# Optimization experiments

Measured on AMD Instinct MI355X. Metric: run time of the kernel, lower is better.

Reference implementation:

```python
import jax, jax.numpy as jnp
import numpy as np

N = 100000   # nodes
E = 1600000  # edges (before self-loops)
IN = 128     # in_dim
H = 32       # hidden (hardcoded in module)
G = 2048     # graphs in batch
NEG_SLOPE = 0.2  # PyG GATConv default leaky_relu slope


def setup_inputs() -> dict:
    key = jax.random.key(0)
    ks = jax.random.split(key, 20)
    inp = {
        "x": jax.random.normal(ks[0], (N, IN), jnp.float32),
        "edge_index": jax.random.randint(ks[1], (2, E), 0, N, dtype=jnp.int64),
        "batch": jnp.sort(jax.random.randint(ks[2], (N,), 0, G, dtype=jnp.int64)),
    }
    dims = [(IN, H), (H, H), (H, H), (H, H)]
    for i, (di, do) in enumerate(dims, start=1):
        k = 3 + 4 * (i - 1)
        inp[f"W{i}"] = jax.random.normal(ks[k], (di, do), jnp.float32) * 0.1
        inp[f"a_s{i}"] = jax.random.normal(ks[k + 1], (do,), jnp.float32) * 0.1
        inp[f"a_d{i}"] = jax.random.normal(ks[k + 2], (do,), jnp.float32) * 0.1
        inp[f"b{i}"] = jnp.zeros((do,), jnp.float32)
    return inp


def _gat(x, src, dst, W, a_s, a_d, b):
    # PyG GATConv, heads=1: h = xW; e_ij = leaky_relu(a_s.h_j + a_d.h_i);
    # alpha = softmax over incoming edges of i; out_i = sum_j alpha_ij * h_j + b
    h = x @ W                                # [N, H]
    es = h @ a_s                             # [N]
    ed = h @ a_d                             # [N]
    e = jax.nn.leaky_relu(es[src] + ed[dst], NEG_SLOPE)   # [E+N]
    m = jax.ops.segment_max(e, dst, num_segments=N)        # per-dest max (stable softmax)
    ex = jnp.exp(e - m[dst])
    denom = jax.ops.segment_sum(ex, dst, num_segments=N)
    alpha = ex / denom[dst]
    out = jax.ops.segment_sum(alpha[:, None] * h[src], dst, num_segments=N)
    return out + b


def reference(x, edge_index, batch, W1, a_s1, a_d1, b1, W2, a_s2, a_d2, b2,
              W3, a_s3, a_d3, b3, W4, a_s4, a_d4, b4):
    # add self-loops once (GATConv add_self_loops=True; same edge set every layer)
    loop = jnp.arange(N, dtype=edge_index.dtype)
    src = jnp.concatenate([edge_index[0], loop])
    dst = jnp.concatenate([edge_index[1], loop])
    x = _gat(x, src, dst, W1, a_s1, a_d1, b1)  # tanh in source is a no-op (result discarded)
    x = _gat(x, src, dst, W2, a_s2, a_d2, b2)
    x = _gat(x, src, dst, W3, a_s3, a_d3, b3)
    x = _gat(x, src, dst, W4, a_s4, a_d4, b4)
    # global_mean_pool
    sums = jax.ops.segment_sum(x, batch, num_segments=G)
    cnt = jax.ops.segment_sum(jnp.ones((N,), x.dtype), batch, num_segments=G)
    return sums / jnp.maximum(cnt, 1.0)[:, None]
```

## Files before the change

### kernel.cpp

```cpp
#include <hip/hip_runtime.h>
#include <hip/hip_fp16.h>

#define HDIM 32
#define IN_DIM 128
#define NEG_SLOPE 0.2f
#define NPB 128
#define NPB_SHIFT 7
#define MAXB 1024
#define CHUNK 8192
#define CAP 4096

typedef _Float16 half8  __attribute__((ext_vector_type(8)));
typedef _Float16 half4v __attribute__((ext_vector_type(4)));
typedef float    floatx4 __attribute__((ext_vector_type(4)));
typedef float    floatx2 __attribute__((ext_vector_type(2)));

__device__ __forceinline__ float leaky(float e) {
    return (e >= 0.f) ? e : NEG_SLOPE * e;
}


template<int K>
__global__ __launch_bounds__(256) void gemm_f32in(
    const float* __restrict__ x, const float* __restrict__ W,
    const float* __restrict__ a_s, const float* __restrict__ a_d,
    uint2* __restrict__ h8, float* __restrict__ es, float* __restrict__ ed, int N)
{
    constexpr int KP = K + 8;
    __shared__ _Float16 xs[64 * KP];
    __shared__ _Float16 Wt[32 * KP];
    __shared__ float stage[64 * 33];
    const int tid = threadIdx.x;
    for (int i = tid; i < K * 32; i += 256) {
        int k = i >> 5, n = i & 31;
        Wt[n * KP + k] = (_Float16)W[i];
    }
    const int lane = tid & 63;
    const int wave = tid >> 6;
    const int m16  = lane & 15;
    const int quad = lane >> 4;
    const float as0 = a_s[m16], as1 = a_s[m16 + 16];
    const float ad0 = a_d[m16], ad1 = a_d[m16 + 16];

    const int ntiles = (N + 63) >> 6;
    for (int tile = blockIdx.x; tile < ntiles; tile += gridDim.x) {
        const int row0 = tile << 6;
        __syncthreads();
        for (int i = tid; i < 64 * (K / 4); i += 256) {
            int r  = i / (K / 4);
            int c4 = i % (K / 4);
            float4 v = (row0 + r < N) ? ((const float4*)x)[(size_t)(row0 + r) * (K / 4) + c4]
                                      : make_float4(0.f, 0.f, 0.f, 0.f);
            half4v hv = { (_Float16)v.x, (_Float16)v.y, (_Float16)v.z, (_Float16)v.w };
            *(half4v*)&xs[r * KP + c4 * 4] = hv;
        }
        __syncthreads();
        floatx4 acc0 = {0.f, 0.f, 0.f, 0.f}, acc1 = {0.f, 0.f, 0.f, 0.f};
        const int rbase = wave * 16;
        #pragma unroll
        for (int kt = 0; kt < K / 32; kt++) {
            half8 a  = *(half8*)&xs[(rbase + m16) * KP + kt * 32 + quad * 8];
            half8 b0 = *(half8*)&Wt[m16 * KP + kt * 32 + quad * 8];
            half8 b1 = *(half8*)&Wt[(m16 + 16) * KP + kt * 32 + quad * 8];
            acc0 = __builtin_amdgcn_mfma_f32_16x16x32_f16(a, b0, acc0, 0, 0, 0);
            acc1 = __builtin_amdgcn_mfma_f32_16x16x32_f16(a, b1, acc1, 0, 0, 0);
        }
        #pragma unroll
        for (int r = 0; r < 4; r++) {
            const int lr = rbase + quad * 4 + r;
            int row = row0 + lr;
            float c0 = acc0[r], c1 = acc1[r];
            stage[lr * 33 + m16]      = c0;
            stage[lr * 33 + m16 + 16] = c1;
            float ps = c0 * as0 + c1 * as1;
            float pd = c0 * ad0 + c1 * ad1;
            #pragma unroll
            for (int m = 8; m >= 1; m >>= 1) { ps += __shfl_xor(ps, m); pd += __shfl_xor(pd, m); }
            if (row < N && m16 == 0) { es[row] = ps; ed[row] = pd; }
        }
        __syncthreads();
        {
            int r = tid >> 2, seg = tid & 3;
            int row = row0 + r;
            if (row < N) {
                const float* sp = &stage[r * 33 + seg * 8];
                unsigned int u0, u1;
                u0 = __builtin_amdgcn_cvt_pk_fp8_f32(sp[0], sp[1], 0,  false);
                u0 = __builtin_amdgcn_cvt_pk_fp8_f32(sp[2], sp[3], u0, true);
                u1 = __builtin_amdgcn_cvt_pk_fp8_f32(sp[4], sp[5], 0,  false);
                u1 = __builtin_amdgcn_cvt_pk_fp8_f32(sp[6], sp[7], u1, true);
                h8[(size_t)row * 4 + seg] = make_uint2(u0, u1);
            }
        }
    }
}


__global__ __launch_bounds__(256) void gemm_f16in(
    const __half* __restrict__ y, const float* __restrict__ W,
    const float* __restrict__ a_s, const float* __restrict__ a_d,
    uint2* __restrict__ h8, float* __restrict__ es, float* __restrict__ ed, int N)
{
    constexpr int K = 32, KP = K + 8;
    __shared__ _Float16 xs[64 * KP];
    __shared__ _Float16 Wt[32 * KP];
    __shared__ float stage[64 * 33];
    const int tid = threadIdx.x;
    {
        int i = tid, k = i >> 5, n = i & 31;
        if (i < K * 32) Wt[n * KP + k] = (_Float16)W[i];
        i = tid + 256; k = i >> 5; n = i & 31;
        if (i < K * 32) Wt[n * KP + k] = (_Float16)W[i];
        i = tid + 512; k = i >> 5; n = i & 31;
        if (i < K * 32) Wt[n * KP + k] = (_Float16)W[i];
        i = tid + 768; k = i >> 5; n = i & 31;
        if (i < K * 32) Wt[n * KP + k] = (_Float16)W[i];
    }
    const int lane = tid & 63;
    const int wave = tid >> 6;
    const int m16  = lane & 15;
    const int quad = lane >> 4;
    const float as0 = a_s[m16], as1 = a_s[m16 + 16];
    const float ad0 = a_d[m16], ad1 = a_d[m16 + 16];

    const int ntiles = (N + 63) >> 6;
    for (int tile = blockIdx.x; tile < ntiles; tile += gridDim.x) {
        const int row0 = tile << 6;
        __syncthreads();
        {
            int r = tid >> 2, c8 = tid & 3;
            int row = row0 + r;
            half8 v;
            if (row < N) v = *(const half8*)((const _Float16*)y + (size_t)row * 32 + c8 * 8);
            else { v = (half8)(_Float16)0.f; }
            *(half8*)&xs[r * KP + c8 * 8] = v;
        }
        __syncthreads();
        floatx4 acc0 = {0.f, 0.f, 0.f, 0.f}, acc1 = {0.f, 0.f, 0.f, 0.f};
        const int rbase = wave * 16;
        half8 a  = *(half8*)&xs[(rbase + m16) * KP + quad * 8];
        half8 b0 = *(half8*)&Wt[m16 * KP + quad * 8];
        half8 b1 = *(half8*)&Wt[(m16 + 16) * KP + quad * 8];
        acc0 = __builtin_amdgcn_mfma_f32_16x16x32_f16(a, b0, acc0, 0, 0, 0);
        acc1 = __builtin_amdgcn_mfma_f32_16x16x32_f16(a, b1, acc1, 0, 0, 0);
        #pragma unroll
        for (int r = 0; r < 4; r++) {
            const int lr = rbase + quad * 4 + r;
            int row = row0 + lr;
            float c0 = acc0[r], c1 = acc1[r];
            stage[lr * 33 + m16]      = c0;
            stage[lr * 33 + m16 + 16] = c1;
            float ps = c0 * as0 + c1 * as1;
            float pd = c0 * ad0 + c1 * ad1;
            #pragma unroll
            for (int m = 8; m >= 1; m >>= 1) { ps += __shfl_xor(ps, m); pd += __shfl_xor(pd, m); }
            if (row < N && m16 == 0) { es[row] = ps; ed[row] = pd; }
        }
        __syncthreads();
        {
            int r = tid >> 2, seg = tid & 3;
            int row = row0 + r;
            if (row < N) {
                const float* sp = &stage[r * 33 + seg * 8];
                unsigned int u0, u1;
                u0 = __builtin_amdgcn_cvt_pk_fp8_f32(sp[0], sp[1], 0,  false);
                u0 = __builtin_amdgcn_cvt_pk_fp8_f32(sp[2], sp[3], u0, true);
                u1 = __builtin_amdgcn_cvt_pk_fp8_f32(sp[4], sp[5], 0,  false);
                u1 = __builtin_amdgcn_cvt_pk_fp8_f32(sp[6], sp[7], u1, true);
                h8[(size_t)row * 4 + seg] = make_uint2(u0, u1);
            }
        }
    }
}


__global__ __launch_bounds__(256) void chunk_hist(
    const int* __restrict__ dsts, int E, int B, int* __restrict__ cnt2D)
{
    __shared__ int hist[MAXB];
    const int blk = blockIdx.x;
    for (int i = threadIdx.x; i < B; i += 256) hist[i] = 0;
    __syncthreads();
    const int e0 = blk * CHUNK;
    for (int i = threadIdx.x; i < CHUNK; i += 256) {
        int e = e0 + i;
        if (e < E) atomicAdd(&hist[dsts[e] >> NPB_SHIFT], 1);
    }
    __syncthreads();
    for (int i = threadIdx.x; i < B; i += 256) cnt2D[(size_t)blk * B + i] = hist[i];
}

__global__ __launch_bounds__(256) void chunk_scan(
    const int* __restrict__ cnt2D, int NBLK, int B,
    int* __restrict__ off2D, int* __restrict__ bcnt)
{
    __shared__ int s[256];
    const int b = blockIdx.x, t = threadIdx.x;
    int v = (t < NBLK) ? cnt2D[(size_t)t * B + b] : 0;
    s[t] = v;
    __syncthreads();
    for (int off = 1; off < 256; off <<= 1) {
        int add = (t >= off) ? s[t - off] : 0;
        __syncthreads();
        s[t] += add;
        __syncthreads();
    }
    if (t < NBLK) off2D[(size_t)t * B + b] = s[t] - v;
    if (t == 255) bcnt[b] = s[255];
}

__global__ __launch_bounds__(1024) void bucket_scan(
    const int* __restrict__ bcnt, int B, int E,
    int* __restrict__ bstart, int* __restrict__ rowptr, int N)
{
    __shared__ int s[1024];
    const int t = threadIdx.x;
    int v = (t < B) ? bcnt[t] : 0;
    s[t] = v;
    __syncthreads();
    for (int off = 1; off < 1024; off <<= 1) {
        int add = (t >= off) ? s[t - off] : 0;
        __syncthreads();
        s[t] += add;
        __syncthreads();
    }
    if (t < B) bstart[t] = s[t] - v;
    if (t == 0) { bstart[B] = E; rowptr[N] = E; }
}

__global__ __launch_bounds__(256) void pair_scatter2(
    const int* __restrict__ srcs, const int* __restrict__ dsts, int E, int B,
    const int* __restrict__ off2D, const int* __restrict__ bstart,
    int* __restrict__ pairs)
{
    __shared__ int cur[MAXB];
    const int blk = blockIdx.x;
    for (int i = threadIdx.x; i < B; i += 256)
        cur[i] = bstart[i] + off2D[(size_t)blk * B + i];
    __syncthreads();
    const int e0 = blk * CHUNK;
    for (int i = threadIdx.x; i < CHUNK; i += 256) {
        int e = e0 + i;
        if (e < E) {
            int s = srcs[e], d = dsts[e];
            int pos = atomicAdd(&cur[d >> NPB_SHIFT], 1);
            pairs[pos] = (s << NPB_SHIFT) | (d & (NPB - 1));
        }
    }
}

__global__ __launch_bounds__(256) void bucket_sort(
    const int* __restrict__ pairs, const int* __restrict__ bstart,
    int* __restrict__ rowptr, int* __restrict__ csrsrc, int N)
{
    __shared__ int ldeg[NPB];
    __shared__ int lex[NPB];
    __shared__ int recs[CAP];
    __shared__ int sorted[CAP];
    const int b = blockIdx.x, t = threadIdx.x;
    const int p0 = bstart[b], p1 = bstart[b + 1];
    const int cnt = p1 - p0;
    if (t < NPB) ldeg[t] = 0;
    __syncthreads();
    for (int i = t; i < cnt; i += 256) {
        int r = pairs[p0 + i];
        atomicAdd(&ldeg[r & (NPB - 1)], 1);
        if (i < CAP) recs[i] = r;
    }
    __syncthreads();
    if (t < NPB) lex[t] = ldeg[t];
    __syncthreads();
    for (int off = 1; off < NPB; off <<= 1) {
        int add = (t >= off && t < NPB) ? lex[t - off] : 0;
        __syncthreads();
        if (t < NPB) lex[t] += add;
        __syncthreads();
    }
    const int node0 = b * NPB;
    if (t < NPB) {
        int excl = lex[t] - ldeg[t];
        if (node0 + t < N) rowptr[node0 + t] = p0 + excl;
        ldeg[t] = excl;
    }
    __syncthreads();
    if (cnt <= CAP) {
        for (int i = t; i < cnt; i += 256) {
            int r = recs[i];
            int pos = atomicAdd(&ldeg[r & (NPB - 1)], 1);
            sorted[pos] = r >> NPB_SHIFT;
        }
        __syncthreads();
        for (int i = t; i < cnt; i += 256) csrsrc[p0 + i] = sorted[i];
    } else {
        for (int i = t; i < cnt; i += 256) {
            int r = pairs[p0 + i];
            int pos = atomicAdd(&ldeg[r & (NPB - 1)], 1);
            csrsrc[p0 + pos] = r >> NPB_SHIFT;
        }
    }
}


__device__ __forceinline__ void acc16(float* acc, uint4 u, float w) {
    floatx2 f0 = __builtin_amdgcn_cvt_pk_f32_fp8(u.x, false);
    floatx2 f1 = __builtin_amdgcn_cvt_pk_f32_fp8(u.x, true);
    floatx2 f2 = __builtin_amdgcn_cvt_pk_f32_fp8(u.y, false);
    floatx2 f3 = __builtin_amdgcn_cvt_pk_f32_fp8(u.y, true);
    floatx2 f4 = __builtin_amdgcn_cvt_pk_f32_fp8(u.z, false);
    floatx2 f5 = __builtin_amdgcn_cvt_pk_f32_fp8(u.z, true);
    floatx2 f6 = __builtin_amdgcn_cvt_pk_f32_fp8(u.w, false);
    floatx2 f7 = __builtin_amdgcn_cvt_pk_f32_fp8(u.w, true);
    acc[0]  += w * f0.x; acc[1]  += w * f0.y; acc[2]  += w * f1.x; acc[3]  += w * f1.y;
    acc[4]  += w * f2.x; acc[5]  += w * f2.y; acc[6]  += w * f3.x; acc[7]  += w * f3.y;
    acc[8]  += w * f4.x; acc[9]  += w * f4.y; acc[10] += w * f5.x; acc[11] += w * f5.y;
    acc[12] += w * f6.x; acc[13] += w * f6.y; acc[14] += w * f7.x; acc[15] += w * f7.y;
}

template<bool LAST>
__global__ __launch_bounds__(256) void agg8(
    const uint4* __restrict__ h8, const float* __restrict__ es, const float* __restrict__ ed,
    const int* __restrict__ rowptr, const int* __restrict__ csrsrc,
    const float* __restrict__ b, __half* __restrict__ y16, float* __restrict__ out, int N)
{
    const int gid  = blockIdx.x * 256 + threadIdx.x;
    const int node = gid >> 1;
    const int l    = threadIdx.x & 1;
    if (node >= N) return;

    const int e0 = rowptr[node];
    const int e1 = rowptr[node + 1];
    const float edi = ed[node];

    float acc[16];
    #pragma unroll
    for (int i = 0; i < 16; i++) acc[i] = 0.f;
    float den = 0.f;

    int e = e0;
    for (; e + 8 <= e1; e += 8) {
        int s[8]; float q[8]; uint4 u[8];
        #pragma unroll
        for (int j = 0; j < 8; j++) s[j] = csrsrc[e + j];
        #pragma unroll
        for (int j = 0; j < 8; j++) q[j] = es[s[j]];
        #pragma unroll
        for (int j = 0; j < 8; j++) u[j] = h8[(size_t)s[j] * 2 + l];
        #pragma unroll
        for (int j = 0; j < 8; j++) {
            float w = __expf(leaky(q[j] + edi));
            den += w;
            acc16(acc, u[j], w);
        }
    }
    for (; e < e1; e++) {
        int s = csrsrc[e];
        float w = __expf(leaky(es[s] + edi));
        uint4 u = h8[(size_t)s * 2 + l];
        den += w;
        acc16(acc, u, w);
    }
    {
        float w = __expf(leaky(es[node] + edi));
        uint4 u = h8[(size_t)node * 2 + l];
        den += w;
        acc16(acc, u, w);
    }

    const float4* b4 = (const float4*)b;
    float inv = 1.f / den;
    float o[16];
    #pragma unroll
    for (int g = 0; g < 4; g++) {
        float4 bv = b4[l * 4 + g];
        o[g*4+0] = acc[g*4+0] * inv + bv.x;
        o[g*4+1] = acc[g*4+1] * inv + bv.y;
        o[g*4+2] = acc[g*4+2] * inv + bv.z;
        o[g*4+3] = acc[g*4+3] * inv + bv.w;
    }

    if (LAST) {
        float4* op = (float4*)out + (size_t)node * 8 + l * 4;
        #pragma unroll
        for (int g = 0; g < 4; g++) {
            float4 v = { o[g*4+0], o[g*4+1], o[g*4+2], o[g*4+3] };
            op[g] = v;
        }
    } else {
        _Float16* yp = (_Float16*)y16 + (size_t)node * 32 + l * 16;
        half8 v0 = { (_Float16)o[0], (_Float16)o[1], (_Float16)o[2], (_Float16)o[3],
                     (_Float16)o[4], (_Float16)o[5], (_Float16)o[6], (_Float16)o[7] };
        half8 v1 = { (_Float16)o[8], (_Float16)o[9], (_Float16)o[10], (_Float16)o[11],
                     (_Float16)o[12], (_Float16)o[13], (_Float16)o[14], (_Float16)o[15] };
        *(half8*)yp = v0;
        *(half8*)(yp + 8) = v1;
    }
}


__global__ __launch_bounds__(256) void pool_graph(
    const float* __restrict__ x, const int* __restrict__ batch,
    float* __restrict__ out, int N, int G)
{
    const int g = (blockIdx.x * 256 + threadIdx.x) >> 6;
    if (g >= G) return;
    const int lane = threadIdx.x & 63;
    const int feat = lane & 31;
    const int half = lane >> 5;

    int lo = 0, hi = N;
    while (lo < hi) { int mid = (lo + hi) >> 1; if (batch[mid] < g) lo = mid + 1; else hi = mid; }
    const int start = lo;
    int lo2 = start, hi2 = N;
    while (lo2 < hi2) { int mid = (lo2 + hi2) >> 1; if (batch[mid] < g + 1) lo2 = mid + 1; else hi2 = mid; }
    const int end = lo2;

    float acc = 0.f;
    for (int i = start + half; i < end; i += 2)
        acc += x[(size_t)i * HDIM + feat];
    acc += __shfl_xor(acc, 32);
    if (half == 0) {
        float cnt = (float)(end - start);
        out[(size_t)g * HDIM + feat] = acc / fmaxf(cnt, 1.f);
    }
}


extern "C" void kernel_launch(void* const* d_in, const int* in_sizes, int n_in,
                              void* d_out, int out_size, void* d_ws, size_t ws_size,
                              hipStream_t stream) {
    const float* x          = (const float*)d_in[0];
    const int*   edge_index = (const int*)d_in[1];
    const int*   batch      = (const int*)d_in[2];

    const int N = in_sizes[2];
    const int E = in_sizes[1] / 2;
    const int G = out_size / HDIM;
    const int B = (N + NPB - 1) / NPB;
    const int NBLK = (E + CHUNK - 1) / CHUNK;
    const int ntiles = (N + 63) / 64;

    const int* srcs = edge_index;
    const int* dsts = edge_index + E;

    char* p = (char*)d_ws;
    uint2* h8     = (uint2*)p; p += (size_t)N * 4 * sizeof(uint2);
    __half* y16   = (__half*)p; p += (size_t)N * HDIM * sizeof(__half);
    float* xbuf   = (float*)p; p += (size_t)N * HDIM * sizeof(float);
    float* es     = (float*)p; p += (size_t)N * sizeof(float);
    float* ed     = (float*)p; p += (size_t)N * sizeof(float);
    int*   rowptr = (int*)p;   p += (size_t)(N + 1) * sizeof(int);
    p += 16 - ((size_t)p & 15);
    int*   csrsrc = (int*)p;   p += (size_t)E * sizeof(int);
    int*   pairs  = (int*)p;   p += (size_t)E * sizeof(int);
    int*   cnt2D  = (int*)p;   p += (size_t)NBLK * B * sizeof(int);
    int*   off2D  = (int*)p;   p += (size_t)NBLK * B * sizeof(int);
    int*   bcnt   = (int*)p;   p += (size_t)B * sizeof(int);
    int*   bstart = (int*)p;   p += (size_t)(B + 1) * sizeof(int);

    chunk_hist  <<<NBLK, 256, 0, stream>>>(dsts, E, B, cnt2D);
    chunk_scan  <<<B, 256, 0, stream>>>(cnt2D, NBLK, B, off2D, bcnt);
    bucket_scan <<<1, 1024, 0, stream>>>(bcnt, B, E, bstart, rowptr, N);
    pair_scatter2<<<NBLK, 256, 0, stream>>>(srcs, dsts, E, B, off2D, bstart, pairs);
    bucket_sort <<<B, 256, 0, stream>>>(pairs, bstart, rowptr, csrsrc, N);

    const int aggGrid = (N * 2 + 255) / 256;

    for (int l = 0; l < 4; l++) {
        const float* W   = (const float*)d_in[3 + 4 * l];
        const float* a_s = (const float*)d_in[4 + 4 * l];
        const float* a_d = (const float*)d_in[5 + 4 * l];
        const float* bb  = (const float*)d_in[6 + 4 * l];

        if (l == 0) gemm_f32in<IN_DIM><<<ntiles, 256, 0, stream>>>(x, W, a_s, a_d, h8, es, ed, N);
        else        gemm_f16in<<<ntiles, 256, 0, stream>>>(y16, W, a_s, a_d, h8, es, ed, N);

        if (l < 3)  agg8<false><<<aggGrid, 256, 0, stream>>>((const uint4*)h8, es, ed, rowptr, csrsrc, bb, y16, xbuf, N);
        else        agg8<true> <<<aggGrid, 256, 0, stream>>>((const uint4*)h8, es, ed, rowptr, csrsrc, bb, y16, xbuf, N);
    }

    pool_graph<<<(G * 64 + 255) / 256, 256, 0, stream>>>(xbuf, batch, (float*)d_out, N, G);
}
```

Measured before the change: 333.4 us.

## Fuse next-layer GEMM and attention projections into aggregation kernel epilogue

The aggregation kernel now also does the next layer's 32x32 linear transform with MFMA in its epilogue. It computes the es/ed attention scores and writes FP8 features directly, using ping-pong buffers. This removes the separate gemm_f16in launch per layer, along with the fp16 intermediate write and re-read of node features. The cost is more shared memory and two block-wide syncs in the aggregation kernel, which may lower occupancy for the latency-bound gather.

```diff
diff --git a/kernel.cpp b/kernel.cpp
--- a/kernel.cpp
+++ b/kernel.cpp
@@ -65,84 +65,6 @@
             acc0 = __builtin_amdgcn_mfma_f32_16x16x32_f16(a, b0, acc0, 0, 0, 0);
             acc1 = __builtin_amdgcn_mfma_f32_16x16x32_f16(a, b1, acc1, 0, 0, 0);
         }
-        #pragma unroll
-        for (int r = 0; r < 4; r++) {
-            const int lr = rbase + quad * 4 + r;
-            int row = row0 + lr;
-            float c0 = acc0[r], c1 = acc1[r];
-            stage[lr * 33 + m16]      = c0;
-            stage[lr * 33 + m16 + 16] = c1;
-            float ps = c0 * as0 + c1 * as1;
-            float pd = c0 * ad0 + c1 * ad1;
-            #pragma unroll
-            for (int m = 8; m >= 1; m >>= 1) { ps += __shfl_xor(ps, m); pd += __shfl_xor(pd, m); }
-            if (row < N && m16 == 0) { es[row] = ps; ed[row] = pd; }
-        }
-        __syncthreads();
-        {
-            int r = tid >> 2, seg = tid & 3;
-            int row = row0 + r;
-            if (row < N) {
-                const float* sp = &stage[r * 33 + seg * 8];
-                unsigned int u0, u1;
-                u0 = __builtin_amdgcn_cvt_pk_fp8_f32(sp[0], sp[1], 0,  false);
-                u0 = __builtin_amdgcn_cvt_pk_fp8_f32(sp[2], sp[3], u0, true);
-                u1 = __builtin_amdgcn_cvt_pk_fp8_f32(sp[4], sp[5], 0,  false);
-                u1 = __builtin_amdgcn_cvt_pk_fp8_f32(sp[6], sp[7], u1, true);
-                h8[(size_t)row * 4 + seg] = make_uint2(u0, u1);
-            }
-        }
-    }
-}
-
-
-__global__ __launch_bounds__(256) void gemm_f16in(
-    const __half* __restrict__ y, const float* __restrict__ W,
-    const float* __restrict__ a_s, const float* __restrict__ a_d,
-    uint2* __restrict__ h8, float* __restrict__ es, float* __restrict__ ed, int N)
-{
-    constexpr int K = 32, KP = K + 8;
-    __shared__ _Float16 xs[64 * KP];
-    __shared__ _Float16 Wt[32 * KP];
-    __shared__ float stage[64 * 33];
-    const int tid = threadIdx.x;
-    {
-        int i = tid, k = i >> 5, n = i & 31;
-        if (i < K * 32) Wt[n * KP + k] = (_Float16)W[i];
-        i = tid + 256; k = i >> 5; n = i & 31;
-        if (i < K * 32) Wt[n * KP + k] = (_Float16)W[i];
-        i = tid + 512; k = i >> 5; n = i & 31;
-        if (i < K * 32) Wt[n * KP + k] = (_Float16)W[i];
-        i = tid + 768; k = i >> 5; n = i & 31;
-        if (i < K * 32) Wt[n * KP + k] = (_Float16)W[i];
-    }
-    const int lane = tid & 63;
-    const int wave = tid >> 6;
-    const int m16  = lane & 15;
-    const int quad = lane >> 4;
-    const float as0 = a_s[m16], as1 = a_s[m16 + 16];
-    const float ad0 = a_d[m16], ad1 = a_d[m16 + 16];
-
-    const int ntiles = (N + 63) >> 6;
-    for (int tile = blockIdx.x; tile < ntiles; tile += gridDim.x) {
-        const int row0 = tile << 6;
-        __syncthreads();
-        {
-            int r = tid >> 2, c8 = tid & 3;
-            int row = row0 + r;
-            half8 v;
-            if (row < N) v = *(const half8*)((const _Float16*)y + (size_t)row * 32 + c8 * 8);
-            else { v = (half8)(_Float16)0.f; }
-            *(half8*)&xs[r * KP + c8 * 8] = v;
-        }
-        __syncthreads();
-        floatx4 acc0 = {0.f, 0.f, 0.f, 0.f}, acc1 = {0.f, 0.f, 0.f, 0.f};
-        const int rbase = wave * 16;
-        half8 a  = *(half8*)&xs[(rbase + m16) * KP + quad * 8];
-        half8 b0 = *(half8*)&Wt[m16 * KP + quad * 8];
-        half8 b1 = *(half8*)&Wt[(m16 + 16) * KP + quad * 8];
-        acc0 = __builtin_amdgcn_mfma_f32_16x16x32_f16(a, b0, acc0, 0, 0, 0);
-        acc1 = __builtin_amdgcn_mfma_f32_16x16x32_f16(a, b1, acc1, 0, 0, 0);
         #pragma unroll
         for (int r = 0; r < 4; r++) {
             const int lr = rbase + quad * 4 + r;
@@ -317,82 +239,159 @@
 }
 
 template<bool LAST>
-__global__ __launch_bounds__(256) void agg8(
-    const uint4* __restrict__ h8, const float* __restrict__ es, const float* __restrict__ ed,
+__global__ __launch_bounds__(256) void agg_mfma(
+    const uint4* __restrict__ h8in, const float* __restrict__ es, const float* __restrict__ ed,
     const int* __restrict__ rowptr, const int* __restrict__ csrsrc,
-    const float* __restrict__ b, __half* __restrict__ y16, float* __restrict__ out, int N)
-{
-    const int gid  = blockIdx.x * 256 + threadIdx.x;
-    const int node = gid >> 1;
-    const int l    = threadIdx.x & 1;
-    if (node >= N) return;
-
-    const int e0 = rowptr[node];
-    const int e1 = rowptr[node + 1];
-    const float edi = ed[node];
+    const float* __restrict__ b,
+    const float* __restrict__ Wn, const float* __restrict__ as_n, const float* __restrict__ ad_n,
+    uint4* __restrict__ h8out, float* __restrict__ es_out, float* __restrict__ ed_out,
+    float* __restrict__ out, int N)
+{
+    constexpr int KP = 40;
+    __shared__ _Float16 xs[128 * KP];
+    __shared__ _Float16 Wt[32 * KP];
+    __shared__ float stage[128 * 33];
+    const int tid = threadIdx.x;
+    if (!LAST) {
+        for (int i = tid; i < 32 * 32; i += 256) {
+            int k = i >> 5, n = i & 31;
+            Wt[n * KP + k] = (_Float16)Wn[i];
+        }
+    }
+    const int node0 = blockIdx.x * 128;
+    const int li    = tid >> 1;
+    const int node  = node0 + li;
+    const int l     = tid & 1;
+    const bool valid = node < N;
 
     float acc[16];
     #pragma unroll
     for (int i = 0; i < 16; i++) acc[i] = 0.f;
     float den = 0.f;
-
-    int e = e0;
-    for (; e + 8 <= e1; e += 8) {
-        int s[8]; float q[8]; uint4 u[8];
-        #pragma unroll
-        for (int j = 0; j < 8; j++) s[j] = csrsrc[e + j];
-        #pragma unroll
-        for (int j = 0; j < 8; j++) q[j] = es[s[j]];
-        #pragma unroll
-        for (int j = 0; j < 8; j++) u[j] = h8[(size_t)s[j] * 2 + l];
-        #pragma unroll
-        for (int j = 0; j < 8; j++) {
-            float w = __expf(leaky(q[j] + edi));
+    float o[16];
+
+    if (valid) {
+        const int e0 = rowptr[node];
+        const int e1 = rowptr[node + 1];
+        const float edi = ed[node];
+        int e = e0;
+        for (; e + 8 <= e1; e += 8) {
+            int s[8]; float q[8]; uint4 u[8];
+            #pragma unroll
+            for (int j = 0; j < 8; j++) s[j] = csrsrc[e + j];
+            #pragma unroll
+            for (int j = 0; j < 8; j++) q[j] = es[s[j]];
+            #pragma unroll
+            for (int j = 0; j < 8; j++) u[j] = h8in[(size_t)s[j] * 2 + l];
+            #pragma unroll
+            for (int j = 0; j < 8; j++) {
+                float w = __expf(leaky(q[j] + edi));
+                den += w;
+                acc16(acc, u[j], w);
+            }
+        }
+        for (; e < e1; e++) {
+            int s = csrsrc[e];
+            float w = __expf(leaky(es[s] + edi));
+            uint4 u = h8in[(size_t)s * 2 + l];
             den += w;
-            acc16(acc, u[j], w);
-        }
-    }
-    for (; e < e1; e++) {
-        int s = csrsrc[e];
-        float w = __expf(leaky(es[s] + edi));
-        uint4 u = h8[(size_t)s * 2 + l];
-        den += w;
-        acc16(acc, u, w);
-    }
-    {
-        float w = __expf(leaky(es[node] + edi));
-        uint4 u = h8[(size_t)node * 2 + l];
-        den += w;
-        acc16(acc, u, w);
-    }
-
-    const float4* b4 = (const float4*)b;
-    float inv = 1.f / den;
-    float o[16];
-    #pragma unroll
-    for (int g = 0; g < 4; g++) {
-        float4 bv = b4[l * 4 + g];
-        o[g*4+0] = acc[g*4+0] * inv + bv.x;
-        o[g*4+1] = acc[g*4+1] * inv + bv.y;
-        o[g*4+2] = acc[g*4+2] * inv + bv.z;
-        o[g*4+3] = acc[g*4+3] * inv + bv.w;
-    }
-
-    if (LAST) {
-        float4* op = (float4*)out + (size_t)node * 8 + l * 4;
+            acc16(acc, u, w);
+        }
+        {
+            float w = __expf(leaky(es[node] + edi));
+            uint4 u = h8in[(size_t)node * 2 + l];
+            den += w;
+            acc16(acc, u, w);
+        }
+        const float4* b4 = (const float4*)b;
+        float inv = 1.f / den;
         #pragma unroll
         for (int g = 0; g < 4; g++) {
-            float4 v = { o[g*4+0], o[g*4+1], o[g*4+2], o[g*4+3] };
-            op[g] = v;
-        }
-    } else {
-        _Float16* yp = (_Float16*)y16 + (size_t)node * 32 + l * 16;
-        half8 v0 = { (_Float16)o[0], (_Float16)o[1], (_Float16)o[2], (_Float16)o[3],
-                     (_Float16)o[4], (_Float16)o[5], (_Float16)o[6], (_Float16)o[7] };
-        half8 v1 = { (_Float16)o[8], (_Float16)o[9], (_Float16)o[10], (_Float16)o[11],
-                     (_Float16)o[12], (_Float16)o[13], (_Float16)o[14], (_Float16)o[15] };
-        *(half8*)yp = v0;
-        *(half8*)(yp + 8) = v1;
+            float4 bv = b4[l * 4 + g];
+            o[g*4+0] = acc[g*4+0] * inv + bv.x;
+            o[g*4+1] = acc[g*4+1] * inv + bv.y;
+            o[g*4+2] = acc[g*4+2] * inv + bv.z;
+            o[g*4+3] = acc[g*4+3] * inv + bv.w;
+        }
+    }
+
+    if (LAST) {
+        if (valid) {
+            float4* op = (float4*)out + (size_t)node * 8 + l * 4;
+            #pragma unroll
+            for (int g = 0; g < 4; g++) {
+                float4 v = { o[g*4+0], o[g*4+1], o[g*4+2], o[g*4+3] };
+                op[g] = v;
+            }
+        }
+        return;
+    }
+
+    {
+        _Float16* xp = &xs[li * KP + l * 16];
+        half8 v0, v1;
+        if (valid) {
+            v0 = (half8){ (_Float16)o[0], (_Float16)o[1], (_Float16)o[2], (_Float16)o[3],
+                          (_Float16)o[4], (_Float16)o[5], (_Float16)o[6], (_Float16)o[7] };
+            v1 = (half8){ (_Float16)o[8], (_Float16)o[9], (_Float16)o[10], (_Float16)o[11],
+                          (_Float16)o[12], (_Float16)o[13], (_Float16)o[14], (_Float16)o[15] };
+        } else {
+            v0 = (half8)(_Float16)0.f;
+            v1 = (half8)(_Float16)0.f;
+        }
+        *(half8*)xp = v0;
+        *(half8*)(xp + 8) = v1;
+    }
+    __syncthreads();
+
+    {
+        const int lane = tid & 63, wave = tid >> 6;
+        const int m16 = lane & 15, quad = lane >> 4;
+        const float as0 = as_n[m16], as1 = as_n[m16 + 16];
+        const float ad0 = ad_n[m16], ad1 = ad_n[m16 + 16];
+        #pragma unroll
+        for (int rt = 0; rt < 2; rt++) {
+            const int rb = wave * 32 + rt * 16;
+            half8 a  = *(half8*)&xs[(rb + m16) * KP + quad * 8];
+            half8 b0 = *(half8*)&Wt[m16 * KP + quad * 8];
+            half8 b1 = *(half8*)&Wt[(m16 + 16) * KP + quad * 8];
+            floatx4 c0 = {0.f,0.f,0.f,0.f}, c1 = {0.f,0.f,0.f,0.f};
+            c0 = __builtin_amdgcn_mfma_f32_16x16x32_f16(a, b0, c0, 0, 0, 0);
+            c1 = __builtin_amdgcn_mfma_f32_16x16x32_f16(a, b1, c1, 0, 0, 0);
+            #pragma unroll
+            for (int r = 0; r < 4; r++) {
+                const int lr = rb + quad * 4 + r;
+                int row = node0 + lr;
+                float v0 = c0[r], v1 = c1[r];
+                stage[lr * 33 + m16]      = v0;
+                stage[lr * 33 + m16 + 16] = v1;
+                float ps = v0 * as0 + v1 * as1;
+                float pd = v0 * ad0 + v1 * ad1;
+                #pragma unroll
+                for (int m = 8; m >= 1; m >>= 1) { ps += __shfl_xor(ps, m); pd += __shfl_xor(pd, m); }
+                if (row < N && m16 == 0) { es_out[row] = ps; ed_out[row] = pd; }
+            }
+        }
+    }
+    __syncthreads();
+
+    {
+        int r = tid >> 1, seg = tid & 1;
+        int row = node0 + r;
+        if (row < N) {
+            const float* sp = &stage[r * 33 + seg * 16];
+            unsigned int u0, u1, u2, u3;
+            u0 = __builtin_amdgcn_cvt_pk_fp8_f32(sp[0],  sp[1],  0,  false);
+            u0 = __builtin_amdgcn_cvt_pk_fp8_f32(sp[2],  sp[3],  u0, true);
+            u1 = __builtin_amdgcn_cvt_pk_fp8_f32(sp[4],  sp[5],  0,  false);
+            u1 = __builtin_amdgcn_cvt_pk_fp8_f32(sp[6],  sp[7],  u1, true);
+            u2 = __builtin_amdgcn_cvt_pk_fp8_f32(sp[8],  sp[9],  0,  false);
+            u2 = __builtin_amdgcn_cvt_pk_fp8_f32(sp[10], sp[11], u2, true);
+            u3 = __builtin_amdgcn_cvt_pk_fp8_f32(sp[12], sp[13], 0,  false);
+            u3 = __builtin_amdgcn_cvt_pk_fp8_f32(sp[14], sp[15], u3, true);
+            uint4 v = { u0, u1, u2, u3 };
+            h8out[(size_t)row * 2 + seg] = v;
+        }
     }
 }
 
@@ -443,11 +442,13 @@
     const int* dsts = edge_index + E;
 
     char* p = (char*)d_ws;
-    uint2* h8     = (uint2*)p; p += (size_t)N * 4 * sizeof(uint2);
-    __half* y16   = (__half*)p; p += (size_t)N * HDIM * sizeof(__half);
+    uint4* h8a    = (uint4*)p; p += (size_t)N * 2 * sizeof(uint4);
+    uint4* h8b    = (uint4*)p; p += (size_t)N * 2 * sizeof(uint4);
     float* xbuf   = (float*)p; p += (size_t)N * HDIM * sizeof(float);
-    float* es     = (float*)p; p += (size_t)N * sizeof(float);
-    float* ed     = (float*)p; p += (size_t)N * sizeof(float);
+    float* esa    = (float*)p; p += (size_t)N * sizeof(float);
+    float* eda    = (float*)p; p += (size_t)N * sizeof(float);
+    float* esb    = (float*)p; p += (size_t)N * sizeof(float);
+    float* edb    = (float*)p; p += (size_t)N * sizeof(float);
     int*   rowptr = (int*)p;   p += (size_t)(N + 1) * sizeof(int);
     p += 16 - ((size_t)p & 15);
     int*   csrsrc = (int*)p;   p += (size_t)E * sizeof(int);
@@ -463,20 +464,34 @@
     pair_scatter2<<<NBLK, 256, 0, stream>>>(srcs, dsts, E, B, off2D, bstart, pairs);
     bucket_sort <<<B, 256, 0, stream>>>(pairs, bstart, rowptr, csrsrc, N);
 
-    const int aggGrid = (N * 2 + 255) / 256;
-
-    for (int l = 0; l < 4; l++) {
-        const float* W   = (const float*)d_in[3 + 4 * l];
-        const float* a_s = (const float*)d_in[4 + 4 * l];
-        const float* a_d = (const float*)d_in[5 + 4 * l];
-        const float* bb  = (const float*)d_in[6 + 4 * l];
-
-        if (l == 0) gemm_f32in<IN_DIM><<<ntiles, 256, 0, stream>>>(x, W, a_s, a_d, h8, es, ed, N);
-        else        gemm_f16in<<<ntiles, 256, 0, stream>>>(y16, W, a_s, a_d, h8, es, ed, N);
-
-        if (l < 3)  agg8<false><<<aggGrid, 256, 0, stream>>>((const uint4*)h8, es, ed, rowptr, csrsrc, bb, y16, xbuf, N);
-        else        agg8<true> <<<aggGrid, 256, 0, stream>>>((const uint4*)h8, es, ed, rowptr, csrsrc, bb, y16, xbuf, N);
-    }
+    const float* W1  = (const float*)d_in[3];
+    const float* as1 = (const float*)d_in[4];
+    const float* ad1 = (const float*)d_in[5];
+    const float* b1  = (const float*)d_in[6];
+    const float* W2  = (const float*)d_in[7];
+    const float* as2 = (const float*)d_in[8];
+    const float* ad2 = (const float*)d_in[9];
+    const float* b2  = (const float*)d_in[10];
+    const float* W3  = (const float*)d_in[11];
+    const float* as3 = (const float*)d_in[12];
+    const float* ad3 = (const float*)d_in[13];
+    const float* b3  = (const float*)d_in[14];
+    const float* W4  = (const float*)d_in[15];
+    const float* as4 = (const float*)d_in[16];
+    const float* ad4 = (const float*)d_in[17];
+    const float* b4  = (const float*)d_in[18];
+
+    const int aggGrid = (N + 127) / 128;
+
+    gemm_f32in<IN_DIM><<<ntiles, 256, 0, stream>>>(x, W1, as1, ad1, (uint2*)h8a, esa, eda, N);
+    agg_mfma<false><<<aggGrid, 256, 0, stream>>>(h8a, esa, eda, rowptr, csrsrc, b1,
+                                                 W2, as2, ad2, h8b, esb, edb, xbuf, N);
+    agg_mfma<false><<<aggGrid, 256, 0, stream>>>(h8b, esb, edb, rowptr, csrsrc, b2,
+                                                 W3, as3, ad3, h8a, esa, eda, xbuf, N);
+    agg_mfma<false><<<aggGrid, 256, 0, stream>>>(h8a, esa, eda, rowptr, csrsrc, b3,
+                                                 W4, as4, ad4, h8b, esb, edb, xbuf, N);
+    agg_mfma<true> <<<aggGrid, 256, 0, stream>>>(h8b, esb, edb, rowptr, csrsrc, b4,
+                                                 W4, as4, ad4, h8a, esa, eda, xbuf, N);
 
     pool_graph<<<(G * 64 + 255) / 256, 256, 0, stream>>>(xbuf, batch, (float*)d_out, N, G);
 }
```

After: 311.4 us. 1.07x faster.
